# Performance work log

Measured on AMD Instinct MI355X. Metric: run time of the kernel, lower is better.

Reference implementation:

```python
import jax, jax.numpy as jnp
import numpy as np

B, S, D = 4, 2048, 1024
E, F, K = 8, 4096, 2  # num_experts, mlp_dim, experts_per_token


def setup_inputs() -> dict:
    key = jax.random.key(0)
    ks = jax.random.split(key, 5)
    scale_d = 1.0 / np.sqrt(D)
    scale_f = 1.0 / np.sqrt(F)
    return {
        "x": jax.random.normal(ks[0], (B, S, D), dtype=jnp.float32),
        "gate_w": jax.random.normal(ks[1], (D, E), dtype=jnp.float32) * scale_d,
        "wi0": jax.random.normal(ks[2], (E, D, F), dtype=jnp.float32) * scale_d,
        "wi1": jax.random.normal(ks[3], (E, D, F), dtype=jnp.float32) * scale_d,
        "wo": jax.random.normal(ks[4], (E, F, D), dtype=jnp.float32) * scale_f,
    }


def reference(x, gate_w, wi0, wi1, wo):
    # Gating: [B,S,E] logits -> top-k values/indices -> softmax over the k selected
    gate_logits = jnp.einsum("bsd,de->bse", x, gate_w)
    topk_w, topk_idx = jax.lax.top_k(gate_logits, K)  # [B,S,K]
    topk_w = jax.nn.softmax(topk_w, axis=-1)

    num_experts = wi0.shape[0]
    out = jnp.zeros_like(x)
    # Faithful to the naive MoE loop: every expert MLP runs over all tokens,
    # output masked/weighted by the token's gate weight for that expert.
    for e in range(num_experts):
        w_e = jnp.sum((topk_idx == e) * topk_w, axis=-1)  # [B,S]
        h = jax.nn.silu(jnp.einsum("bsd,df->bsf", x, wi0[e])) * jnp.einsum(
            "bsd,df->bsf", x, wi1[e]
        )  # gated SiLU MLP intermediate [B,S,F]
        out = out + w_e[..., None] * jnp.einsum("bsf,fd->bsd", h, wo[e])
    return out
```

## Files before the change

### kernel.cpp

```cpp
#include <hip/hip_runtime.h>
#include <math.h>

#define TOKENS 8192
#define DDIM 1024
#define FDIM 4096
#define NEXP 8
#define CAP 8192
#define BM 128
#define BN 128
#define BK 64

typedef __bf16 bf16x8 __attribute__((ext_vector_type(8)));
typedef float f32x4 __attribute__((ext_vector_type(4)));

__device__ __forceinline__ unsigned short f2bf(float f) {
  union { float f; unsigned int u; } v; v.f = f;
  unsigned int u = v.u;
  return (unsigned short)((u + 0x7FFFu + ((u >> 16) & 1u)) >> 16);
}
__device__ __forceinline__ float bf2f(unsigned short h) {
  union { unsigned int u; float f; } v; v.u = ((unsigned int)h) << 16;
  return v.f;
}

__device__ __forceinline__ void load_lds16(const void* g, void* l) {
  __builtin_amdgcn_global_load_lds(
      (const __attribute__((address_space(1))) void*)g,
      (__attribute__((address_space(3))) void*)l, 16, 0, 0);
}

__global__ void k_tconv(const float* __restrict__ in, unsigned short* __restrict__ out,
                        int R, int C) {
  __shared__ float tile[32][132];
  size_t mat = (size_t)R * C;
  const float* src = in + (size_t)blockIdx.z * mat;
  unsigned short* dst = out + (size_t)blockIdx.z * mat;
  int c0 = blockIdx.x * 128, r0 = blockIdx.y * 32;
  int t = threadIdx.x;
#pragma unroll
  for (int i = 0; i < 4; ++i) {
    int idx = i * 1024 + t * 4;
    int r = idx >> 7, c = idx & 127;
    float4 v = *(const float4*)(src + (size_t)(r0 + r) * C + (c0 + c));
    *(float4*)&tile[r][c] = v;
  }
  __syncthreads();
#pragma unroll
  for (int i = 0; i < 4; ++i) {
    int idx = i * 1024 + t * 4;
    int c = idx >> 5, r = idx & 31;
    ushort4 o;
    o.x = f2bf(tile[r + 0][c]);
    o.y = f2bf(tile[r + 1][c]);
    o.z = f2bf(tile[r + 2][c]);
    o.w = f2bf(tile[r + 3][c]);
    *(ushort4*)(dst + (size_t)(c0 + c) * R + (r0 + r)) = o;
  }
}


__global__ void k_zero(int* __restrict__ counts) {
  if (threadIdx.x < NEXP) counts[threadIdx.x] = 0;
}

__global__ void k_gate(const float* __restrict__ x, const float* __restrict__ gw,
                       unsigned short* __restrict__ xb,
                       int* __restrict__ counts, int* __restrict__ tok_list,
                       float* __restrict__ wgt_list, int* __restrict__ tok_slot) {
  int wave = threadIdx.x >> 6, lane = threadIdx.x & 63;
  int t = blockIdx.x * 4 + wave;
  const float* xr = x + (size_t)t * DDIM;
  unsigned short* xbr = xb + (size_t)t * DDIM;
  float acc[NEXP];
#pragma unroll
  for (int e = 0; e < NEXP; ++e) acc[e] = 0.f;
  for (int d = lane; d < DDIM; d += 64) {
    float xv = xr[d];
    xbr[d] = f2bf(xv);
    const float* g = gw + d * NEXP;
#pragma unroll
    for (int e = 0; e < NEXP; ++e) acc[e] += xv * g[e];
  }
#pragma unroll
  for (int e = 0; e < NEXP; ++e) {
#pragma unroll
    for (int off = 32; off > 0; off >>= 1) acc[e] += __shfl_down(acc[e], off, 64);
  }
  if (lane == 0) {
    int e0 = 0; float v0 = acc[0];
#pragma unroll
    for (int e = 1; e < NEXP; ++e) if (acc[e] > v0) { v0 = acc[e]; e0 = e; }
    int e1 = -1; float v1 = -3.0e38f;
#pragma unroll
    for (int e = 0; e < NEXP; ++e) if (e != e0 && acc[e] > v1) { v1 = acc[e]; e1 = e; }
    float p1 = expf(v1 - v0);
    float s = 1.0f + p1;
    float w0 = 1.0f / s, w1 = p1 / s;
    int pos0 = atomicAdd(&counts[e0], 1);
    tok_list[e0 * CAP + pos0] = t;
    wgt_list[e0 * CAP + pos0] = w0;
    tok_slot[t * 2 + 0] = e0 * CAP + pos0;
    int pos1 = atomicAdd(&counts[e1], 1);
    tok_list[e1 * CAP + pos1] = t;
    wgt_list[e1 * CAP + pos1] = w1;
    tok_slot[t * 2 + 1] = e1 * CAP + pos1;
  }
}

__global__ void k_scan(const int* __restrict__ counts, int* __restrict__ bases) {
  if (threadIdx.x == 0) {
    int s = 0;
    for (int e = 0; e < NEXP; ++e) { bases[e] = s; s += counts[e]; }
  }
}



__global__ __launch_bounds__(256, 2) void k_gemm1(
    const unsigned short* __restrict__ xb, const unsigned short* __restrict__ w0t,
    const unsigned short* __restrict__ w1t, const int* __restrict__ counts,
    const int* __restrict__ bases, const int* __restrict__ tok_list,
    unsigned short* __restrict__ H) {
  int b = blockIdx.x;
  int xcd = b & 7, j = b >> 3;
  int i8 = j & 7, grp = j >> 3;
  int G = grp * 8 + xcd;
  int e = G >> 8;
  int mt = (G >> 2) & 63;
  int nt = ((G & 3) << 3) | i8;

  int cnt = counts[e];
  int m0 = mt * BM;
  if (m0 >= cnt) return;
  int mv = min(BM, cnt - m0);
  int gbase = bases[e] + m0;

  __shared__ __align__(16) unsigned short As[BM * BK];
  __shared__ __align__(16) unsigned short B0s[BN * BK];
  __shared__ __align__(16) unsigned short B1s[BN * BK];
  __shared__ int toks[BM];

  int t = threadIdx.x;
  if (t < BM) toks[t] = tok_list[e * CAP + m0 + min(t, mv - 1)];
  __syncthreads();

  int wid = t >> 6, lane = t & 63;
  int wm = (wid >> 1) * 64, wn = (wid & 1) * 64;
  int fr = lane & 15, fq = lane >> 4;
  int sw = fr & 7;
  int co0 = (fq ^ sw) * 8;
  int co1 = ((4 | fq) ^ sw) * 8;

  int srow[4], soff[4];
#pragma unroll
  for (int r = 0; r < 4; ++r) {
    int s = t + r * 256;
    srow[r] = s >> 3;
    soff[r] = ((s & 7) ^ (srow[r] & 7)) * 8;
  }
  size_t arow[4];
#pragma unroll
  for (int r = 0; r < 4; ++r) arow[r] = (size_t)toks[srow[r]] * DDIM + soff[r];

  f32x4 acc0[4][4], acc1[4][4];
#pragma unroll
  for (int mi = 0; mi < 4; ++mi)
#pragma unroll
    for (int ni = 0; ni < 4; ++ni)
#pragma unroll
      for (int r = 0; r < 4; ++r) { acc0[mi][ni][r] = 0.f; acc1[mi][ni][r] = 0.f; }

  const unsigned short* b0p = w0t + ((size_t)e * FDIM + nt * BN) * DDIM;
  const unsigned short* b1p = w1t + ((size_t)e * FDIM + nt * BN) * DDIM;

  for (int kt = 0; kt < DDIM; kt += BK) {
#pragma unroll
    for (int r = 0; r < 4; ++r) {
      int s = t + r * 256;
      load_lds16(xb + arow[r] + kt, As + s * 8);
      load_lds16(b0p + (size_t)srow[r] * DDIM + soff[r] + kt, B0s + s * 8);
      load_lds16(b1p + (size_t)srow[r] * DDIM + soff[r] + kt, B1s + s * 8);
    }
    __syncthreads();
#pragma unroll
    for (int kh = 0; kh < 2; ++kh) {
      int co = kh ? co1 : co0;
      bf16x8 a[4], b0[4], b1[4];
#pragma unroll
      for (int mi = 0; mi < 4; ++mi)
        a[mi] = *(const bf16x8*)(As + (wm + mi * 16 + fr) * BK + co);
#pragma unroll
      for (int ni = 0; ni < 4; ++ni) {
        b0[ni] = *(const bf16x8*)(B0s + (wn + ni * 16 + fr) * BK + co);
        b1[ni] = *(const bf16x8*)(B1s + (wn + ni * 16 + fr) * BK + co);
      }
#pragma unroll
      for (int mi = 0; mi < 4; ++mi)
#pragma unroll
        for (int ni = 0; ni < 4; ++ni) {
          acc0[mi][ni] = __builtin_amdgcn_mfma_f32_16x16x32_bf16(a[mi], b0[ni], acc0[mi][ni], 0, 0, 0);
          acc1[mi][ni] = __builtin_amdgcn_mfma_f32_16x16x32_bf16(a[mi], b1[ni], acc1[mi][ni], 0, 0, 0);
        }
    }
    __syncthreads();
  }

  int n0 = nt * BN + wn;
#pragma unroll
  for (int mi = 0; mi < 4; ++mi) {
    int mloc = wm + mi * 16 + fq * 4;
#pragma unroll
    for (int ni = 0; ni < 4; ++ni) {
      int col = n0 + ni * 16 + fr;
#pragma unroll
      for (int r = 0; r < 4; ++r) {
        int mrow = mloc + r;
        if (mrow < mv) {
          float g = acc0[mi][ni][r];
          float hv = (g / (1.0f + expf(-g))) * acc1[mi][ni][r];
          H[(size_t)(gbase + mrow) * FDIM + col] = f2bf(hv);
        }
      }
    }
  }
}


__global__ __launch_bounds__(256, 2) void k_gemm2(
    const unsigned short* __restrict__ H, const unsigned short* __restrict__ wot,
    const int* __restrict__ counts, const int* __restrict__ bases,
    unsigned short* __restrict__ O) {
  int b = blockIdx.x;
  int xcd = b & 7, j = b >> 3;
  int i8 = j & 7, grp = j >> 3;
  int G = grp * 8 + xcd;
  int e = G >> 6;
  int mt = G & 63;
  int nt = i8;

  int cnt = counts[e];
  int m0 = mt * BM;
  if (m0 >= cnt) return;
  int mv = min(BM, cnt - m0);
  int gbase = bases[e] + m0;

  __shared__ __align__(16) unsigned short As[BM * BK];
  __shared__ __align__(16) unsigned short Bs[BN * BK];

  int t = threadIdx.x;
  int wid = t >> 6, lane = t & 63;
  int wm = (wid >> 1) * 64, wn = (wid & 1) * 64;
  int fr = lane & 15, fq = lane >> 4;
  int sw = fr & 7;
  int co0 = (fq ^ sw) * 8;
  int co1 = ((4 | fq) ^ sw) * 8;

  int srow[4], soff[4];
#pragma unroll
  for (int r = 0; r < 4; ++r) {
    int s = t + r * 256;
    srow[r] = s >> 3;
    soff[r] = ((s & 7) ^ (srow[r] & 7)) * 8;
  }
  size_t arow[4];
#pragma unroll
  for (int r = 0; r < 4; ++r)
    arow[r] = (size_t)(gbase + min(srow[r], mv - 1)) * FDIM + soff[r];

  f32x4 acc[4][4];
#pragma unroll
  for (int mi = 0; mi < 4; ++mi)
#pragma unroll
    for (int ni = 0; ni < 4; ++ni)
#pragma unroll
      for (int r = 0; r < 4; ++r) acc[mi][ni][r] = 0.f;

  const unsigned short* bp = wot + ((size_t)e * DDIM + nt * BN) * FDIM;

  for (int kt = 0; kt < FDIM; kt += BK) {
#pragma unroll
    for (int r = 0; r < 4; ++r) {
      int s = t + r * 256;
      load_lds16(H + arow[r] + kt, As + s * 8);
      load_lds16(bp + (size_t)srow[r] * FDIM + soff[r] + kt, Bs + s * 8);
    }
    __syncthreads();
#pragma unroll
    for (int kh = 0; kh < 2; ++kh) {
      int co = kh ? co1 : co0;
      bf16x8 a[4], bb[4];
#pragma unroll
      for (int mi = 0; mi < 4; ++mi)
        a[mi] = *(const bf16x8*)(As + (wm + mi * 16 + fr) * BK + co);
#pragma unroll
      for (int ni = 0; ni < 4; ++ni)
        bb[ni] = *(const bf16x8*)(Bs + (wn + ni * 16 + fr) * BK + co);
#pragma unroll
      for (int mi = 0; mi < 4; ++mi)
#pragma unroll
        for (int ni = 0; ni < 4; ++ni)
          acc[mi][ni] = __builtin_amdgcn_mfma_f32_16x16x32_bf16(a[mi], bb[ni], acc[mi][ni], 0, 0, 0);
    }
    __syncthreads();
  }

  int n0 = nt * BN + wn;
#pragma unroll
  for (int mi = 0; mi < 4; ++mi) {
    int mloc = wm + mi * 16 + fq * 4;
#pragma unroll
    for (int ni = 0; ni < 4; ++ni) {
      int col = n0 + ni * 16 + fr;
#pragma unroll
      for (int r = 0; r < 4; ++r) {
        int mrow = mloc + r;
        if (mrow < mv)
          O[(size_t)(gbase + mrow) * DDIM + col] = f2bf(acc[mi][ni][r]);
      }
    }
  }
}


__global__ void k_combine(const unsigned short* __restrict__ O, const int* __restrict__ bases,
                          const int* __restrict__ tok_slot, const float* __restrict__ wgt_list,
                          float* __restrict__ out) {
  int t = blockIdx.x;
  int s0 = tok_slot[t * 2 + 0];
  int s1 = tok_slot[t * 2 + 1];
  int g0 = bases[s0 / CAP] + (s0 & (CAP - 1));
  int g1 = bases[s1 / CAP] + (s1 & (CAP - 1));
  float w0 = wgt_list[s0], w1 = wgt_list[s1];
  int d = threadIdx.x * 4;
  ushort4 a = *(const ushort4*)(O + (size_t)g0 * DDIM + d);
  ushort4 b = *(const ushort4*)(O + (size_t)g1 * DDIM + d);
  float4 r;
  r.x = w0 * bf2f(a.x) + w1 * bf2f(b.x);
  r.y = w0 * bf2f(a.y) + w1 * bf2f(b.y);
  r.z = w0 * bf2f(a.z) + w1 * bf2f(b.z);
  r.w = w0 * bf2f(a.w) + w1 * bf2f(b.w);
  *(float4*)(out + (size_t)t * DDIM + d) = r;
}


extern "C" void kernel_launch(void* const* d_in, const int* in_sizes, int n_in,
                              void* d_out, int out_size, void* d_ws, size_t ws_size,
                              hipStream_t stream) {
  const float* x   = (const float*)d_in[0];
  const float* gw  = (const float*)d_in[1];
  const float* wi0 = (const float*)d_in[2];
  const float* wi1 = (const float*)d_in[3];
  const float* wo  = (const float*)d_in[4];
  float* out = (float*)d_out;

  char* p = (char*)d_ws;
  unsigned short* xb  = (unsigned short*)p; p += (size_t)TOKENS * DDIM * 2;
  unsigned short* w0t = (unsigned short*)p; p += (size_t)NEXP * FDIM * DDIM * 2;
  unsigned short* w1t = (unsigned short*)p; p += (size_t)NEXP * FDIM * DDIM * 2;
  unsigned short* wot = (unsigned short*)p; p += (size_t)NEXP * DDIM * FDIM * 2;
  unsigned short* H   = (unsigned short*)p; p += (size_t)2 * TOKENS * FDIM * 2;
  unsigned short* O   = (unsigned short*)p; p += (size_t)2 * TOKENS * DDIM * 2;
  int*   counts   = (int*)p; p += 256;
  int*   bases    = (int*)p; p += 256;
  int*   tok_list = (int*)p; p += (size_t)NEXP * CAP * 4;
  float* wgt_list = (float*)p; p += (size_t)NEXP * CAP * 4;
  int*   tok_slot = (int*)p; p += (size_t)TOKENS * 2 * 4;

  k_tconv<<<dim3(FDIM / 128, DDIM / 32, NEXP), 256, 0, stream>>>(wi0, w0t, DDIM, FDIM);
  k_tconv<<<dim3(FDIM / 128, DDIM / 32, NEXP), 256, 0, stream>>>(wi1, w1t, DDIM, FDIM);
  k_tconv<<<dim3(DDIM / 128, FDIM / 32, NEXP), 256, 0, stream>>>(wo, wot, FDIM, DDIM);

  k_zero<<<1, 64, 0, stream>>>(counts);
  k_gate<<<TOKENS / 4, 256, 0, stream>>>(x, gw, xb, counts, tok_list, wgt_list, tok_slot);
  k_scan<<<1, 64, 0, stream>>>(counts, bases);

  k_gemm1<<<(FDIM / BN) * (CAP / BM) * NEXP, 256, 0, stream>>>(xb, w0t, w1t, counts, bases, tok_list, H);
  k_gemm2<<<(DDIM / BN) * (CAP / BM) * NEXP, 256, 0, stream>>>(H, wot, counts, bases, O);

  k_combine<<<TOKENS, 256, 0, stream>>>(O, bases, tok_slot, wgt_list, out);
}
```

Before: 1.164 ms.

## Pipeline expert GEMMs with 4-stage LDS ring and larger 512-thread tiles

Both expert GEMMs move from a single-buffered load-then-compute loop with two barriers per K-step to a 4-slot LDS ring with K=32 slices. Loads run three stages ahead, and progress is gated by explicit vmcnt waits plus one barrier per step. Tiles grow (256x128 for gemm1, 256x256 for gemm2) with 512-thread blocks, and MFMA sections are wrapped in setprio. This hides global-load latency and improves operand reuse, at the cost of more LDS, higher register pressure, and coarser tiles that waste more work on partially filled expert tiles.

```diff
diff --git a/kernel.cpp b/kernel.cpp
--- a/kernel.cpp
+++ b/kernel.cpp
@@ -6,9 +6,13 @@
 #define FDIM 4096
 #define NEXP 8
 #define CAP 8192
-#define BM 128
-#define BN 128
-#define BK 64
+#define TK 32
+#define BM1 256
+#define BN1 128
+#define NT1 (DDIM / TK)
+#define BM2 256
+#define BN2 256
+#define NT2 (FDIM / TK)
 
 typedef __bf16 bf16x8 __attribute__((ext_vector_type(8)));
 typedef float f32x4 __attribute__((ext_vector_type(4)));
@@ -28,6 +32,9 @@
       (const __attribute__((address_space(1))) void*)g,
       (__attribute__((address_space(3))) void*)l, 16, 0, 0);
 }
+
+#define VMW(n) asm volatile("s_waitcnt vmcnt(" #n ")" ::: "memory")
+#define BARRIER() do { __builtin_amdgcn_s_barrier(); asm volatile("" ::: "memory"); } while (0)
 
 __global__ void k_tconv(const float* __restrict__ in, unsigned short* __restrict__ out,
                         int R, int C) {
@@ -116,7 +123,7 @@
 
 
 
-__global__ __launch_bounds__(256, 2) void k_gemm1(
+__global__ __launch_bounds__(512, 2) void k_gemm1(
     const unsigned short* __restrict__ xb, const unsigned short* __restrict__ w0t,
     const unsigned short* __restrict__ w1t, const int* __restrict__ counts,
     const int* __restrict__ bases, const int* __restrict__ tok_list,
@@ -125,42 +132,47 @@
   int xcd = b & 7, j = b >> 3;
   int i8 = j & 7, grp = j >> 3;
   int G = grp * 8 + xcd;
-  int e = G >> 8;
-  int mt = (G >> 2) & 63;
+  int e = G >> 7;
+  int mt = (G >> 2) & 31;
   int nt = ((G & 3) << 3) | i8;
 
   int cnt = counts[e];
-  int m0 = mt * BM;
+  int m0 = mt * BM1;
   if (m0 >= cnt) return;
-  int mv = min(BM, cnt - m0);
+  int mv = min(BM1, cnt - m0);
   int gbase = bases[e] + m0;
 
-  __shared__ __align__(16) unsigned short As[BM * BK];
-  __shared__ __align__(16) unsigned short B0s[BN * BK];
-  __shared__ __align__(16) unsigned short B1s[BN * BK];
-  __shared__ int toks[BM];
+  __shared__ __align__(16) unsigned short As[4][BM1 * TK];
+  __shared__ __align__(16) unsigned short B0s[4][BN1 * TK];
+  __shared__ __align__(16) unsigned short B1s[4][BN1 * TK];
+  __shared__ int toks[BM1];
 
   int t = threadIdx.x;
-  if (t < BM) toks[t] = tok_list[e * CAP + m0 + min(t, mv - 1)];
+  if (t < BM1) toks[t] = tok_list[e * CAP + m0 + min(t, mv - 1)];
   __syncthreads();
 
   int wid = t >> 6, lane = t & 63;
   int wm = (wid >> 1) * 64, wn = (wid & 1) * 64;
   int fr = lane & 15, fq = lane >> 4;
-  int sw = fr & 7;
-  int co0 = (fq ^ sw) * 8;
-  int co1 = ((4 | fq) ^ sw) * 8;
-
-  int srow[4], soff[4];
-#pragma unroll
-  for (int r = 0; r < 4; ++r) {
-    int s = t + r * 256;
-    srow[r] = s >> 3;
-    soff[r] = ((s & 7) ^ (srow[r] & 7)) * 8;
-  }
-  size_t arow[4];
-#pragma unroll
-  for (int r = 0; r < 4; ++r) arow[r] = (size_t)toks[srow[r]] * DDIM + soff[r];
+  int co = (fq ^ (fr & 3)) * 8;
+
+  const unsigned short* b0p = w0t + ((size_t)e * FDIM + (size_t)nt * BN1) * DDIM;
+  const unsigned short* b1p = w1t + ((size_t)e * FDIM + (size_t)nt * BN1) * DDIM;
+
+  const unsigned short *srcA0, *srcA1;
+  int ldsA0, ldsA1;
+  {
+    int s0 = t, s1 = t + 512;
+    int r0 = s0 >> 2, r1 = s1 >> 2;
+    srcA0 = xb + (size_t)toks[r0] * DDIM + ((s0 & 3) ^ (r0 & 3)) * 8;
+    srcA1 = xb + (size_t)toks[r1] * DDIM + ((s1 & 3) ^ (r1 & 3)) * 8;
+    ldsA0 = s0 * 8; ldsA1 = s1 * 8;
+  }
+  int rb = t >> 2;
+  int sbo = ((t & 3) ^ (rb & 3)) * 8;
+  const unsigned short* srcB0 = b0p + (size_t)rb * DDIM + sbo;
+  const unsigned short* srcB1 = b1p + (size_t)rb * DDIM + sbo;
+  int ldsB = t * 8;
 
   f32x4 acc0[4][4], acc1[4][4];
 #pragma unroll
@@ -170,42 +182,43 @@
 #pragma unroll
       for (int r = 0; r < 4; ++r) { acc0[mi][ni][r] = 0.f; acc1[mi][ni][r] = 0.f; }
 
-  const unsigned short* b0p = w0t + ((size_t)e * FDIM + nt * BN) * DDIM;
-  const unsigned short* b1p = w1t + ((size_t)e * FDIM + nt * BN) * DDIM;
-
-  for (int kt = 0; kt < DDIM; kt += BK) {
-#pragma unroll
-    for (int r = 0; r < 4; ++r) {
-      int s = t + r * 256;
-      load_lds16(xb + arow[r] + kt, As + s * 8);
-      load_lds16(b0p + (size_t)srow[r] * DDIM + soff[r] + kt, B0s + s * 8);
-      load_lds16(b1p + (size_t)srow[r] * DDIM + soff[r] + kt, B1s + s * 8);
-    }
-    __syncthreads();
-#pragma unroll
-    for (int kh = 0; kh < 2; ++kh) {
-      int co = kh ? co1 : co0;
-      bf16x8 a[4], b0[4], b1[4];
-#pragma unroll
-      for (int mi = 0; mi < 4; ++mi)
-        a[mi] = *(const bf16x8*)(As + (wm + mi * 16 + fr) * BK + co);
-#pragma unroll
-      for (int ni = 0; ni < 4; ++ni) {
-        b0[ni] = *(const bf16x8*)(B0s + (wn + ni * 16 + fr) * BK + co);
-        b1[ni] = *(const bf16x8*)(B1s + (wn + ni * 16 + fr) * BK + co);
-      }
-#pragma unroll
-      for (int mi = 0; mi < 4; ++mi)
-#pragma unroll
-        for (int ni = 0; ni < 4; ++ni) {
-          acc0[mi][ni] = __builtin_amdgcn_mfma_f32_16x16x32_bf16(a[mi], b0[ni], acc0[mi][ni], 0, 0, 0);
-          acc1[mi][ni] = __builtin_amdgcn_mfma_f32_16x16x32_bf16(a[mi], b1[ni], acc1[mi][ni], 0, 0, 0);
-        }
-    }
-    __syncthreads();
-  }
-
-  int n0 = nt * BN + wn;
+#define STAGE1(kt, sl) do { int c_ = (kt) * TK;          \
+    load_lds16(srcA0 + c_, &As[sl][ldsA0]);              \
+    load_lds16(srcA1 + c_, &As[sl][ldsA1]);              \
+    load_lds16(srcB0 + c_, &B0s[sl][ldsB]);              \
+    load_lds16(srcB1 + c_, &B1s[sl][ldsB]); } while (0)
+
+#define COMPUTE1(sl) do {                                                   \
+    const unsigned short* ap = As[sl];                                      \
+    const unsigned short* q0 = B0s[sl];                                     \
+    const unsigned short* q1 = B1s[sl];                                     \
+    bf16x8 a[4], p0[4], p1[4];                                              \
+    _Pragma("unroll") for (int mi = 0; mi < 4; ++mi)                        \
+      a[mi] = *(const bf16x8*)(ap + (wm + mi * 16 + fr) * TK + co);         \
+    _Pragma("unroll") for (int ni = 0; ni < 4; ++ni) {                      \
+      p0[ni] = *(const bf16x8*)(q0 + (wn + ni * 16 + fr) * TK + co);        \
+      p1[ni] = *(const bf16x8*)(q1 + (wn + ni * 16 + fr) * TK + co); }      \
+    __builtin_amdgcn_s_setprio(1);                                          \
+    _Pragma("unroll") for (int mi = 0; mi < 4; ++mi)                        \
+      _Pragma("unroll") for (int ni = 0; ni < 4; ++ni) {                    \
+        acc0[mi][ni] = __builtin_amdgcn_mfma_f32_16x16x32_bf16(a[mi], p0[ni], acc0[mi][ni], 0, 0, 0); \
+        acc1[mi][ni] = __builtin_amdgcn_mfma_f32_16x16x32_bf16(a[mi], p1[ni], acc1[mi][ni], 0, 0, 0); } \
+    __builtin_amdgcn_s_setprio(0); } while (0)
+
+  STAGE1(0, 0); STAGE1(1, 1); STAGE1(2, 2);
+  for (int kt = 0; kt < NT1 - 3; ++kt) {
+    VMW(8);
+    BARRIER();
+    STAGE1(kt + 3, (kt + 3) & 3);
+    COMPUTE1(kt & 3);
+  }
+  VMW(8); BARRIER(); COMPUTE1((NT1 - 3) & 3);
+  VMW(4); BARRIER(); COMPUTE1((NT1 - 2) & 3);
+  VMW(0); BARRIER(); COMPUTE1((NT1 - 1) & 3);
+#undef STAGE1
+#undef COMPUTE1
+
+  int n0 = nt * BN1 + wn;
 #pragma unroll
   for (int mi = 0; mi < 4; ++mi) {
     int mloc = wm + mi * 16 + fq * 4;
@@ -226,7 +239,7 @@
 }
 
 
-__global__ __launch_bounds__(256, 2) void k_gemm2(
+__global__ __launch_bounds__(512, 2) void k_gemm2(
     const unsigned short* __restrict__ H, const unsigned short* __restrict__ wot,
     const int* __restrict__ counts, const int* __restrict__ bases,
     unsigned short* __restrict__ O) {
@@ -234,79 +247,85 @@
   int xcd = b & 7, j = b >> 3;
   int i8 = j & 7, grp = j >> 3;
   int G = grp * 8 + xcd;
-  int e = G >> 6;
-  int mt = G & 63;
-  int nt = i8;
+  int e = G >> 4;
+  int nt = (G >> 2) & 3;
+  int mt = ((G & 3) << 3) | i8;
 
   int cnt = counts[e];
-  int m0 = mt * BM;
+  int m0 = mt * BM2;
   if (m0 >= cnt) return;
-  int mv = min(BM, cnt - m0);
+  int mv = min(BM2, cnt - m0);
   int gbase = bases[e] + m0;
 
-  __shared__ __align__(16) unsigned short As[BM * BK];
-  __shared__ __align__(16) unsigned short Bs[BN * BK];
+  __shared__ __align__(16) unsigned short As[4][BM2 * TK];
+  __shared__ __align__(16) unsigned short Bs[4][BN2 * TK];
 
   int t = threadIdx.x;
   int wid = t >> 6, lane = t & 63;
-  int wm = (wid >> 1) * 64, wn = (wid & 1) * 64;
+  int wm = (wid >> 2) * 128, wn = (wid & 3) * 64;
   int fr = lane & 15, fq = lane >> 4;
-  int sw = fr & 7;
-  int co0 = (fq ^ sw) * 8;
-  int co1 = ((4 | fq) ^ sw) * 8;
-
-  int srow[4], soff[4];
-#pragma unroll
-  for (int r = 0; r < 4; ++r) {
-    int s = t + r * 256;
-    srow[r] = s >> 3;
-    soff[r] = ((s & 7) ^ (srow[r] & 7)) * 8;
-  }
-  size_t arow[4];
-#pragma unroll
-  for (int r = 0; r < 4; ++r)
-    arow[r] = (size_t)(gbase + min(srow[r], mv - 1)) * FDIM + soff[r];
-
-  f32x4 acc[4][4];
-#pragma unroll
-  for (int mi = 0; mi < 4; ++mi)
+  int co = (fq ^ (fr & 3)) * 8;
+
+  const unsigned short* bp = wot + ((size_t)e * DDIM + (size_t)nt * BN2) * FDIM;
+
+  const unsigned short *srcA0, *srcA1, *srcB0, *srcB1;
+  int ldsA0, ldsA1, ldsB0, ldsB1;
+  {
+    int s0 = t, s1 = t + 512;
+    int r0 = s0 >> 2, r1 = s1 >> 2;
+    int o0 = ((s0 & 3) ^ (r0 & 3)) * 8, o1 = ((s1 & 3) ^ (r1 & 3)) * 8;
+    srcA0 = H + (size_t)(gbase + min(r0, mv - 1)) * FDIM + o0;
+    srcA1 = H + (size_t)(gbase + min(r1, mv - 1)) * FDIM + o1;
+    srcB0 = bp + (size_t)r0 * FDIM + o0;
+    srcB1 = bp + (size_t)r1 * FDIM + o1;
+    ldsA0 = s0 * 8; ldsA1 = s1 * 8;
+    ldsB0 = s0 * 8; ldsB1 = s1 * 8;
+  }
+
+  f32x4 acc[8][4];
+#pragma unroll
+  for (int mi = 0; mi < 8; ++mi)
 #pragma unroll
     for (int ni = 0; ni < 4; ++ni)
 #pragma unroll
       for (int r = 0; r < 4; ++r) acc[mi][ni][r] = 0.f;
 
-  const unsigned short* bp = wot + ((size_t)e * DDIM + nt * BN) * FDIM;
-
-  for (int kt = 0; kt < FDIM; kt += BK) {
-#pragma unroll
-    for (int r = 0; r < 4; ++r) {
-      int s = t + r * 256;
-      load_lds16(H + arow[r] + kt, As + s * 8);
-      load_lds16(bp + (size_t)srow[r] * FDIM + soff[r] + kt, Bs + s * 8);
-    }
-    __syncthreads();
-#pragma unroll
-    for (int kh = 0; kh < 2; ++kh) {
-      int co = kh ? co1 : co0;
-      bf16x8 a[4], bb[4];
-#pragma unroll
-      for (int mi = 0; mi < 4; ++mi)
-        a[mi] = *(const bf16x8*)(As + (wm + mi * 16 + fr) * BK + co);
-#pragma unroll
-      for (int ni = 0; ni < 4; ++ni)
-        bb[ni] = *(const bf16x8*)(Bs + (wn + ni * 16 + fr) * BK + co);
-#pragma unroll
-      for (int mi = 0; mi < 4; ++mi)
-#pragma unroll
-        for (int ni = 0; ni < 4; ++ni)
-          acc[mi][ni] = __builtin_amdgcn_mfma_f32_16x16x32_bf16(a[mi], bb[ni], acc[mi][ni], 0, 0, 0);
-    }
-    __syncthreads();
-  }
-
-  int n0 = nt * BN + wn;
-#pragma unroll
-  for (int mi = 0; mi < 4; ++mi) {
+#define STAGE2(kt, sl) do { int c_ = (kt) * TK;          \
+    load_lds16(srcA0 + c_, &As[sl][ldsA0]);              \
+    load_lds16(srcA1 + c_, &As[sl][ldsA1]);              \
+    load_lds16(srcB0 + c_, &Bs[sl][ldsB0]);              \
+    load_lds16(srcB1 + c_, &Bs[sl][ldsB1]); } while (0)
+
+#define COMPUTE2(sl) do {                                                   \
+    const unsigned short* ap = As[sl];                                      \
+    const unsigned short* qp = Bs[sl];                                      \
+    bf16x8 a[8], p[4];                                                      \
+    _Pragma("unroll") for (int mi = 0; mi < 8; ++mi)                        \
+      a[mi] = *(const bf16x8*)(ap + (wm + mi * 16 + fr) * TK + co);         \
+    _Pragma("unroll") for (int ni = 0; ni < 4; ++ni)                        \
+      p[ni] = *(const bf16x8*)(qp + (wn + ni * 16 + fr) * TK + co);         \
+    __builtin_amdgcn_s_setprio(1);                                          \
+    _Pragma("unroll") for (int mi = 0; mi < 8; ++mi)                        \
+      _Pragma("unroll") for (int ni = 0; ni < 4; ++ni)                      \
+        acc[mi][ni] = __builtin_amdgcn_mfma_f32_16x16x32_bf16(a[mi], p[ni], acc[mi][ni], 0, 0, 0); \
+    __builtin_amdgcn_s_setprio(0); } while (0)
+
+  STAGE2(0, 0); STAGE2(1, 1); STAGE2(2, 2);
+  for (int kt = 0; kt < NT2 - 3; ++kt) {
+    VMW(8);
+    BARRIER();
+    STAGE2(kt + 3, (kt + 3) & 3);
+    COMPUTE2(kt & 3);
+  }
+  VMW(8); BARRIER(); COMPUTE2((NT2 - 3) & 3);
+  VMW(4); BARRIER(); COMPUTE2((NT2 - 2) & 3);
+  VMW(0); BARRIER(); COMPUTE2((NT2 - 1) & 3);
+#undef STAGE2
+#undef COMPUTE2
+
+  int n0 = nt * BN2 + wn;
+#pragma unroll
+  for (int mi = 0; mi < 8; ++mi) {
     int mloc = wm + mi * 16 + fq * 4;
 #pragma unroll
     for (int ni = 0; ni < 4; ++ni) {
@@ -374,8 +393,8 @@
   k_gate<<<TOKENS / 4, 256, 0, stream>>>(x, gw, xb, counts, tok_list, wgt_list, tok_slot);
   k_scan<<<1, 64, 0, stream>>>(counts, bases);
 
-  k_gemm1<<<(FDIM / BN) * (CAP / BM) * NEXP, 256, 0, stream>>>(xb, w0t, w1t, counts, bases, tok_list, H);
-  k_gemm2<<<(DDIM / BN) * (CAP / BM) * NEXP, 256, 0, stream>>>(H, wot, counts, bases, O);
+  k_gemm1<<<NEXP * (CAP / BM1) * (FDIM / BN1), 512, 0, stream>>>(xb, w0t, w1t, counts, bases, tok_list, H);
+  k_gemm2<<<NEXP * (CAP / BM2) * (DDIM / BN2), 512, 0, stream>>>(H, wot, counts, bases, O);
 
   k_combine<<<TOKENS, 256, 0, stream>>>(O, bases, tok_slot, wgt_list, out);
 }
```

Result: slower. 1.783 ms (+53.2%).

## Multi-buffer LDS pipeline in MoE GEMMs with 512-thread blocks

Applied to the files above, without the earlier changes.

Both expert GEMM kernels now use 8 waves per block instead of 4, with each wave owning a 64x32 subtile. They also replace the load-sync-compute-sync loop with a 3-stage (gemm1) or 4-stage (gemm2) LDS ring buffer that uses explicit vmcnt waits and a single barrier per iteration. MFMA sections are wrapped in s_setprio to favour compute issue. The aim is to overlap global-to-LDS loads with MFMA work and cut barrier stalls. The cost is much more LDS per block (about 144KB for gemm1 and 128KB for gemm2), which may limit occupancy to one block per CU despite launch_bounds(512,2).

```diff
diff --git a/kernel.cpp b/kernel.cpp
--- a/kernel.cpp
+++ b/kernel.cpp
@@ -9,6 +9,8 @@
 #define BM 128
 #define BN 128
 #define BK 64
+#define NT1 (DDIM / BK)
+#define NT2 (FDIM / BK)
 
 typedef __bf16 bf16x8 __attribute__((ext_vector_type(8)));
 typedef float f32x4 __attribute__((ext_vector_type(4)));
@@ -28,6 +30,11 @@
       (const __attribute__((address_space(1))) void*)g,
       (__attribute__((address_space(3))) void*)l, 16, 0, 0);
 }
+
+#define VMW(n) asm volatile("s_waitcnt vmcnt(" #n ")" ::: "memory")
+#define BARRIER() do { asm volatile("" ::: "memory"); \
+                       __builtin_amdgcn_s_barrier();  \
+                       asm volatile("" ::: "memory"); } while (0)
 
 __global__ void k_tconv(const float* __restrict__ in, unsigned short* __restrict__ out,
                         int R, int C) {
@@ -116,7 +123,7 @@
 
 
 
-__global__ __launch_bounds__(256, 2) void k_gemm1(
+__global__ __launch_bounds__(512, 2) void k_gemm1(
     const unsigned short* __restrict__ xb, const unsigned short* __restrict__ w0t,
     const unsigned short* __restrict__ w1t, const int* __restrict__ counts,
     const int* __restrict__ bases, const int* __restrict__ tok_list,
@@ -135,9 +142,9 @@
   int mv = min(BM, cnt - m0);
   int gbase = bases[e] + m0;
 
-  __shared__ __align__(16) unsigned short As[BM * BK];
-  __shared__ __align__(16) unsigned short B0s[BN * BK];
-  __shared__ __align__(16) unsigned short B1s[BN * BK];
+  __shared__ __align__(16) unsigned short As[3][BM * BK];
+  __shared__ __align__(16) unsigned short B0s[3][BM * BK];
+  __shared__ __align__(16) unsigned short B1s[3][BM * BK];
   __shared__ int toks[BM];
 
   int t = threadIdx.x;
@@ -145,72 +152,82 @@
   __syncthreads();
 
   int wid = t >> 6, lane = t & 63;
-  int wm = (wid >> 1) * 64, wn = (wid & 1) * 64;
+  int wm = (wid >> 2) * 64, wn = (wid & 3) * 32;
   int fr = lane & 15, fq = lane >> 4;
   int sw = fr & 7;
   int co0 = (fq ^ sw) * 8;
   int co1 = ((4 | fq) ^ sw) * 8;
 
-  int srow[4], soff[4];
-#pragma unroll
-  for (int r = 0; r < 4; ++r) {
-    int s = t + r * 256;
-    srow[r] = s >> 3;
-    soff[r] = ((s & 7) ^ (srow[r] & 7)) * 8;
-  }
-  size_t arow[4];
-#pragma unroll
-  for (int r = 0; r < 4; ++r) arow[r] = (size_t)toks[srow[r]] * DDIM + soff[r];
-
-  f32x4 acc0[4][4], acc1[4][4];
+  const unsigned short* b0p = w0t + ((size_t)e * FDIM + (size_t)nt * BN) * DDIM;
+  const unsigned short* b1p = w1t + ((size_t)e * FDIM + (size_t)nt * BN) * DDIM;
+
+  int s0 = t, s1 = t + 512;
+  int r0 = s0 >> 3, r1 = s1 >> 3;
+  int o0 = ((s0 & 7) ^ (r0 & 7)) * 8, o1 = ((s1 & 7) ^ (r1 & 7)) * 8;
+  const unsigned short* pA0 = xb + (size_t)toks[r0] * DDIM + o0;
+  const unsigned short* pA1 = xb + (size_t)toks[r1] * DDIM + o1;
+  const unsigned short* pB00 = b0p + (size_t)r0 * DDIM + o0;
+  const unsigned short* pB01 = b0p + (size_t)r1 * DDIM + o1;
+  const unsigned short* pB10 = b1p + (size_t)r0 * DDIM + o0;
+  const unsigned short* pB11 = b1p + (size_t)r1 * DDIM + o1;
+
+  f32x4 acc0[4][2], acc1[4][2];
 #pragma unroll
   for (int mi = 0; mi < 4; ++mi)
 #pragma unroll
-    for (int ni = 0; ni < 4; ++ni)
+    for (int ni = 0; ni < 2; ++ni)
 #pragma unroll
       for (int r = 0; r < 4; ++r) { acc0[mi][ni][r] = 0.f; acc1[mi][ni][r] = 0.f; }
 
-  const unsigned short* b0p = w0t + ((size_t)e * FDIM + nt * BN) * DDIM;
-  const unsigned short* b1p = w1t + ((size_t)e * FDIM + nt * BN) * DDIM;
-
-  for (int kt = 0; kt < DDIM; kt += BK) {
-#pragma unroll
-    for (int r = 0; r < 4; ++r) {
-      int s = t + r * 256;
-      load_lds16(xb + arow[r] + kt, As + s * 8);
-      load_lds16(b0p + (size_t)srow[r] * DDIM + soff[r] + kt, B0s + s * 8);
-      load_lds16(b1p + (size_t)srow[r] * DDIM + soff[r] + kt, B1s + s * 8);
-    }
-    __syncthreads();
-#pragma unroll
-    for (int kh = 0; kh < 2; ++kh) {
-      int co = kh ? co1 : co0;
-      bf16x8 a[4], b0[4], b1[4];
-#pragma unroll
-      for (int mi = 0; mi < 4; ++mi)
-        a[mi] = *(const bf16x8*)(As + (wm + mi * 16 + fr) * BK + co);
-#pragma unroll
-      for (int ni = 0; ni < 4; ++ni) {
-        b0[ni] = *(const bf16x8*)(B0s + (wn + ni * 16 + fr) * BK + co);
-        b1[ni] = *(const bf16x8*)(B1s + (wn + ni * 16 + fr) * BK + co);
-      }
-#pragma unroll
-      for (int mi = 0; mi < 4; ++mi)
-#pragma unroll
-        for (int ni = 0; ni < 4; ++ni) {
-          acc0[mi][ni] = __builtin_amdgcn_mfma_f32_16x16x32_bf16(a[mi], b0[ni], acc0[mi][ni], 0, 0, 0);
-          acc1[mi][ni] = __builtin_amdgcn_mfma_f32_16x16x32_bf16(a[mi], b1[ni], acc1[mi][ni], 0, 0, 0);
-        }
-    }
-    __syncthreads();
-  }
+#define STAGE1(kt, sl) do { int c_ = (kt) * BK;         \
+    load_lds16(pA0 + c_,  &As[sl][s0 * 8]);             \
+    load_lds16(pA1 + c_,  &As[sl][s1 * 8]);             \
+    load_lds16(pB00 + c_, &B0s[sl][s0 * 8]);            \
+    load_lds16(pB01 + c_, &B0s[sl][s1 * 8]);            \
+    load_lds16(pB10 + c_, &B1s[sl][s0 * 8]);            \
+    load_lds16(pB11 + c_, &B1s[sl][s1 * 8]); } while (0)
+
+#define COMPUTE1(sl) do {                                                   \
+    const unsigned short* ap = As[sl];                                      \
+    const unsigned short* q0 = B0s[sl];                                     \
+    const unsigned short* q1 = B1s[sl];                                     \
+    bf16x8 a[2][4], b0[2][2], b1[2][2];                                     \
+    _Pragma("unroll") for (int mi = 0; mi < 4; ++mi) {                      \
+      a[0][mi] = *(const bf16x8*)(ap + (wm + mi * 16 + fr) * BK + co0);     \
+      a[1][mi] = *(const bf16x8*)(ap + (wm + mi * 16 + fr) * BK + co1); }   \
+    _Pragma("unroll") for (int ni = 0; ni < 2; ++ni) {                      \
+      b0[0][ni] = *(const bf16x8*)(q0 + (wn + ni * 16 + fr) * BK + co0);    \
+      b0[1][ni] = *(const bf16x8*)(q0 + (wn + ni * 16 + fr) * BK + co1);    \
+      b1[0][ni] = *(const bf16x8*)(q1 + (wn + ni * 16 + fr) * BK + co0);    \
+      b1[1][ni] = *(const bf16x8*)(q1 + (wn + ni * 16 + fr) * BK + co1); }  \
+    __builtin_amdgcn_s_setprio(1);                                          \
+    _Pragma("unroll") for (int kh = 0; kh < 2; ++kh)                        \
+      _Pragma("unroll") for (int mi = 0; mi < 4; ++mi)                      \
+        _Pragma("unroll") for (int ni = 0; ni < 2; ++ni) {                  \
+          acc0[mi][ni] = __builtin_amdgcn_mfma_f32_16x16x32_bf16(a[kh][mi], b0[kh][ni], acc0[mi][ni], 0, 0, 0); \
+          acc1[mi][ni] = __builtin_amdgcn_mfma_f32_16x16x32_bf16(a[kh][mi], b1[kh][ni], acc1[mi][ni], 0, 0, 0); } \
+    __builtin_amdgcn_s_setprio(0); } while (0)
+
+  STAGE1(0, 0);
+  STAGE1(1, 1);
+  int cur = 0, nxt = 2;
+  for (int kt = 0; kt < NT1; ++kt) {
+    if (kt < NT1 - 1) { VMW(6); } else { VMW(0); }
+    BARRIER();
+    if (kt + 2 < NT1) STAGE1(kt + 2, nxt);
+    COMPUTE1(cur);
+    cur = (cur == 2) ? 0 : cur + 1;
+    nxt = (nxt == 2) ? 0 : nxt + 1;
+  }
+#undef STAGE1
+#undef COMPUTE1
 
   int n0 = nt * BN + wn;
 #pragma unroll
   for (int mi = 0; mi < 4; ++mi) {
     int mloc = wm + mi * 16 + fq * 4;
 #pragma unroll
-    for (int ni = 0; ni < 4; ++ni) {
+    for (int ni = 0; ni < 2; ++ni) {
       int col = n0 + ni * 16 + fr;
 #pragma unroll
       for (int r = 0; r < 4; ++r) {
@@ -226,7 +243,7 @@
 }
 
 
-__global__ __launch_bounds__(256, 2) void k_gemm2(
+__global__ __launch_bounds__(512, 2) void k_gemm2(
     const unsigned short* __restrict__ H, const unsigned short* __restrict__ wot,
     const int* __restrict__ counts, const int* __restrict__ bases,
     unsigned short* __restrict__ O) {
@@ -244,72 +261,78 @@
   int mv = min(BM, cnt - m0);
   int gbase = bases[e] + m0;
 
-  __shared__ __align__(16) unsigned short As[BM * BK];
-  __shared__ __align__(16) unsigned short Bs[BN * BK];
+  __shared__ __align__(16) unsigned short As[4][BM * BK];
+  __shared__ __align__(16) unsigned short Bs[4][BN * BK];
 
   int t = threadIdx.x;
   int wid = t >> 6, lane = t & 63;
-  int wm = (wid >> 1) * 64, wn = (wid & 1) * 64;
+  int wm = (wid >> 2) * 64, wn = (wid & 3) * 32;
   int fr = lane & 15, fq = lane >> 4;
   int sw = fr & 7;
   int co0 = (fq ^ sw) * 8;
   int co1 = ((4 | fq) ^ sw) * 8;
 
-  int srow[4], soff[4];
-#pragma unroll
-  for (int r = 0; r < 4; ++r) {
-    int s = t + r * 256;
-    srow[r] = s >> 3;
-    soff[r] = ((s & 7) ^ (srow[r] & 7)) * 8;
-  }
-  size_t arow[4];
-#pragma unroll
-  for (int r = 0; r < 4; ++r)
-    arow[r] = (size_t)(gbase + min(srow[r], mv - 1)) * FDIM + soff[r];
-
-  f32x4 acc[4][4];
+  const unsigned short* bp = wot + ((size_t)e * DDIM + (size_t)nt * BN) * FDIM;
+
+  int s0 = t, s1 = t + 512;
+  int r0 = s0 >> 3, r1 = s1 >> 3;
+  int o0 = ((s0 & 7) ^ (r0 & 7)) * 8, o1 = ((s1 & 7) ^ (r1 & 7)) * 8;
+  const unsigned short* pA0 = H + (size_t)(gbase + min(r0, mv - 1)) * FDIM + o0;
+  const unsigned short* pA1 = H + (size_t)(gbase + min(r1, mv - 1)) * FDIM + o1;
+  const unsigned short* pB0 = bp + (size_t)r0 * FDIM + o0;
+  const unsigned short* pB1 = bp + (size_t)r1 * FDIM + o1;
+
+  f32x4 acc[4][2];
 #pragma unroll
   for (int mi = 0; mi < 4; ++mi)
 #pragma unroll
-    for (int ni = 0; ni < 4; ++ni)
+    for (int ni = 0; ni < 2; ++ni)
 #pragma unroll
       for (int r = 0; r < 4; ++r) acc[mi][ni][r] = 0.f;
 
-  const unsigned short* bp = wot + ((size_t)e * DDIM + nt * BN) * FDIM;
-
-  for (int kt = 0; kt < FDIM; kt += BK) {
-#pragma unroll
-    for (int r = 0; r < 4; ++r) {
-      int s = t + r * 256;
-      load_lds16(H + arow[r] + kt, As + s * 8);
-      load_lds16(bp + (size_t)srow[r] * FDIM + soff[r] + kt, Bs + s * 8);
-    }
-    __syncthreads();
-#pragma unroll
-    for (int kh = 0; kh < 2; ++kh) {
-      int co = kh ? co1 : co0;
-      bf16x8 a[4], bb[4];
-#pragma unroll
-      for (int mi = 0; mi < 4; ++mi)
-        a[mi] = *(const bf16x8*)(As + (wm + mi * 16 + fr) * BK + co);
-#pragma unroll
-      for (int ni = 0; ni < 4; ++ni)
-        bb[ni] = *(const bf16x8*)(Bs + (wn + ni * 16 + fr) * BK + co);
-#pragma unroll
-      for (int mi = 0; mi < 4; ++mi)
-#pragma unroll
-        for (int ni = 0; ni < 4; ++ni)
-          acc[mi][ni] = __builtin_amdgcn_mfma_f32_16x16x32_bf16(a[mi], bb[ni], acc[mi][ni], 0, 0, 0);
-    }
-    __syncthreads();
-  }
+#define STAGE2(kt, sl) do { int c_ = (kt) * BK;         \
+    load_lds16(pA0 + c_, &As[sl][s0 * 8]);              \
+    load_lds16(pA1 + c_, &As[sl][s1 * 8]);              \
+    load_lds16(pB0 + c_, &Bs[sl][s0 * 8]);              \
+    load_lds16(pB1 + c_, &Bs[sl][s1 * 8]); } while (0)
+
+#define COMPUTE2(sl) do {                                                   \
+    const unsigned short* ap = As[sl];                                      \
+    const unsigned short* qp = Bs[sl];                                      \
+    bf16x8 a[2][4], bb[2][2];                                               \
+    _Pragma("unroll") for (int mi = 0; mi < 4; ++mi) {                      \
+      a[0][mi] = *(const bf16x8*)(ap + (wm + mi * 16 + fr) * BK + co0);     \
+      a[1][mi] = *(const bf16x8*)(ap + (wm + mi * 16 + fr) * BK + co1); }   \
+    _Pragma("unroll") for (int ni = 0; ni < 2; ++ni) {                      \
+      bb[0][ni] = *(const bf16x8*)(qp + (wn + ni * 16 + fr) * BK + co0);    \
+      bb[1][ni] = *(const bf16x8*)(qp + (wn + ni * 16 + fr) * BK + co1); }  \
+    __builtin_amdgcn_s_setprio(1);                                          \
+    _Pragma("unroll") for (int kh = 0; kh < 2; ++kh)                        \
+      _Pragma("unroll") for (int mi = 0; mi < 4; ++mi)                      \
+        _Pragma("unroll") for (int ni = 0; ni < 2; ++ni)                    \
+          acc[mi][ni] = __builtin_amdgcn_mfma_f32_16x16x32_bf16(a[kh][mi], bb[kh][ni], acc[mi][ni], 0, 0, 0); \
+    __builtin_amdgcn_s_setprio(0); } while (0)
+
+  STAGE2(0, 0);
+  STAGE2(1, 1);
+  STAGE2(2, 2);
+  for (int kt = 0; kt < NT2; ++kt) {
+    if (kt <= NT2 - 3) { VMW(8); }
+    else if (kt == NT2 - 2) { VMW(4); }
+    else { VMW(0); }
+    BARRIER();
+    if (kt + 3 < NT2) STAGE2(kt + 3, (kt + 3) & 3);
+    COMPUTE2(kt & 3);
+  }
+#undef STAGE2
+#undef COMPUTE2
 
   int n0 = nt * BN + wn;
 #pragma unroll
   for (int mi = 0; mi < 4; ++mi) {
     int mloc = wm + mi * 16 + fq * 4;
 #pragma unroll
-    for (int ni = 0; ni < 4; ++ni) {
+    for (int ni = 0; ni < 2; ++ni) {
       int col = n0 + ni * 16 + fr;
 #pragma unroll
       for (int r = 0; r < 4; ++r) {
@@ -374,8 +397,8 @@
   k_gate<<<TOKENS / 4, 256, 0, stream>>>(x, gw, xb, counts, tok_list, wgt_list, tok_slot);
   k_scan<<<1, 64, 0, stream>>>(counts, bases);
 
-  k_gemm1<<<(FDIM / BN) * (CAP / BM) * NEXP, 256, 0, stream>>>(xb, w0t, w1t, counts, bases, tok_list, H);
-  k_gemm2<<<(DDIM / BN) * (CAP / BM) * NEXP, 256, 0, stream>>>(H, wot, counts, bases, O);
+  k_gemm1<<<(FDIM / BN) * (CAP / BM) * NEXP, 512, 0, stream>>>(xb, w0t, w1t, counts, bases, tok_list, H);
+  k_gemm2<<<(DDIM / BN) * (CAP / BM) * NEXP, 512, 0, stream>>>(H, wot, counts, bases, O);
 
   k_combine<<<TOKENS, 256, 0, stream>>>(O, bases, tok_slot, wgt_list, out);
 }
```

After: 1.437 ms. 1.24x slower.
